# Performance work log

Measured on AMD Instinct MI355X. Metric: run time of the kernel, lower is better.

## Reference

```python
import jax, jax.numpy as jnp
import numpy as np

PATCH = 32        # max_patch_size == patch_stride == gate dim
LEVELS = 3        # n_real_experts; patch sizes 32 -> 16 -> 8
N_REAL = 3
N_NULL = 1
N_EXPERTS = N_REAL + N_NULL
K = 2             # n_activated_experts
ROUTE_SCALE = 1.0
SEQ_LEN = 2097152


def setup_inputs():
    key = jax.random.key(0)
    kx, kw = jax.random.split(key)
    x = jax.random.normal(kx, (1, SEQ_LEN), dtype=jnp.float32)
    mask = jnp.ones((1, SEQ_LEN), dtype=jnp.float32)
    Wg = jax.random.normal(kw, (N_EXPERTS, PATCH), dtype=jnp.float32) * 0.02
    return {"x": x, "mask": mask, "Wg": Wg}


def _route_structure(scores_np):
    """Concrete (non-differentiable) routing / split structure.
    scores_np: [P, E] gate softmax scores. Returns top-k ids, parent map,
    gather positions, validity mask, final sizes, granularity mask."""
    idx = np.argsort(-scores_np, axis=-1)[:, :K]                 # top-k expert ids [P,K]
    masked = np.where(idx < N_REAL, idx, -1)
    lvl = masked.max(axis=-1)
    lvl = np.maximum(lvl, 0)                                     # null-expert-only -> level 0
    counts = (1 << lvl).astype(np.int64)                         # each patch -> 2**lvl children
    P = scores_np.shape[0]
    total = int(counts.sum())
    parent = np.repeat(np.arange(P), counts)                     # [T] original patch id
    starts = np.cumsum(counts) - counts
    c = np.arange(total) - np.repeat(starts, counts)             # chunk index within parent
    v = lvl[parent]                                              # split level of each final patch
    sz = (PATCH >> v).astype(np.int64)                           # final patch length
    t = np.arange(PATCH)[None, :]
    valid = (t < sz[:, None])
    pos = np.where(valid, c[:, None] * sz[:, None] + t, 0)       # gather offsets in parent block
    # granularity mask: ones at own chunk at own level, and containing chunk one level coarser
    g = np.zeros((total, LEVELS, PATCH), np.float32)
    own = ((t >= (c * sz)[:, None]) & (t < ((c + 1) * sz)[:, None])).astype(np.float32)
    g[np.arange(total), v] = own
    hp = v >= 1
    szp = PATCH >> np.maximum(v - 1, 0)
    cp = c // 2
    par = ((t >= (cp * szp)[:, None]) & (t < ((cp + 1) * szp)[:, None])).astype(np.float32)
    g[np.arange(total)[hp], (v - 1)[hp]] = par[hp]
    return idx, parent, pos, valid, sz, g


def reference(x, mask, Wg):
    # non-overlapping patchify (stride == patch size)
    xp = x.reshape(-1, PATCH)                                    # [P, PATCH]
    mp = mask.reshape(-1, PATCH)
    scores = jax.nn.softmax(xp @ Wg.T, axis=-1)                  # [P, E] gate scores
    idx_np, parent, pos, valid, sz, g = _route_structure(np.asarray(scores))
    idx = jnp.asarray(idx_np)
    w_top = jnp.take_along_axis(scores, idx, axis=-1) * ROUTE_SCALE   # [P, K]
    parent_j = jnp.asarray(parent)
    pos_j = jnp.asarray(pos)
    valid_f = jnp.asarray(valid.astype(np.float32))
    xg = xp[parent_j]                                            # parent blocks [T, PATCH]
    mg = mp[parent_j]                                            # parent block masks
    new_x = jnp.take_along_axis(xg, pos_j, axis=1) * valid_f     # left-aligned, zero padded
    new_mask = jnp.take_along_axis(mg, pos_j, axis=1) * valid_f
    new_size = jnp.asarray(sz.astype(np.int32))                  # [T]
    weights = w_top[parent_j]                                    # children inherit routing [T,K]
    expert_idx = idx[parent_j]                                   # [T,K]
    gran = jnp.asarray(g)                                        # [T, LEVELS, PATCH]
    x_final = xg[:, None, :] * gran * mg[:, None, :]             # [T, LEVELS, PATCH]
    return (new_x[None], new_mask[None], new_size[None],
            weights[None], expert_idx[None], x_final[None])
```

## Files before the change

### kernel.cpp

```cpp
#include <hip/hip_runtime.h>

#define PATCH 32

__global__ __launch_bounds__(256) void k_gate(
    const float* __restrict__ x, const float* __restrict__ Wg,
    float* __restrict__ w0o, float* __restrict__ w1o,
    int* __restrict__ meta, int* __restrict__ lstart,
    int* __restrict__ blockSums)
{
    __shared__ float sx[256 * 33];
    __shared__ float sw[128];
    __shared__ int   sc[256];
    const int tid = threadIdx.x;
    const long base = (long)blockIdx.x * (256 * PATCH);

    for (int k = tid; k < 256 * PATCH; k += 256)
        sx[(k >> 5) * 33 + (k & 31)] = x[base + k];
    if (tid < 128) sw[tid] = Wg[tid];
    __syncthreads();

    const float* xp = &sx[tid * 33];
    float z0 = 0.f, z1 = 0.f, z2 = 0.f, z3 = 0.f;
    #pragma unroll
    for (int i = 0; i < 32; i++) {
        const float xv = xp[i];
        z0 = fmaf(xv, sw[i],      z0);
        z1 = fmaf(xv, sw[32 + i], z1);
        z2 = fmaf(xv, sw[64 + i], z2);
        z3 = fmaf(xv, sw[96 + i], z3);
    }
    const float zm = fmaxf(fmaxf(z0, z1), fmaxf(z2, z3));
    const float e0 = expf(z0 - zm), e1 = expf(z1 - zm),
                e2 = expf(z2 - zm), e3 = expf(z3 - zm);
    const float s = e0 + e1 + e2 + e3;
    float pv[4];
    pv[0] = e0 / s; pv[1] = e1 / s; pv[2] = e2 / s; pv[3] = e3 / s;

    int b0 = 0; float v0 = pv[0];
    #pragma unroll
    for (int i = 1; i < 4; i++) if (pv[i] > v0) { v0 = pv[i]; b0 = i; }
    int b1 = -1; float v1 = -1.f;
    #pragma unroll
    for (int i = 0; i < 4; i++) if (i != b0 && pv[i] > v1) { v1 = pv[i]; b1 = i; }

    const int m0 = (b0 < 3) ? b0 : -1;
    const int m1 = (b1 < 3) ? b1 : -1;
    int lv = m0 > m1 ? m0 : m1;
    if (lv < 0) lv = 0;
    const int cnt = 1 << lv;

    const int gp = blockIdx.x * 256 + tid;
    w0o[gp] = v0;
    w1o[gp] = v1;
    meta[gp] = b0 | (b1 << 4) | (lv << 8);

    sc[tid] = cnt;
    __syncthreads();
    for (int off = 1; off < 256; off <<= 1) {
        const int t = (tid >= off) ? sc[tid - off] : 0;
        __syncthreads();
        sc[tid] += t;
        __syncthreads();
    }
    lstart[gp] = sc[tid] - cnt;
    if (tid == 255) blockSums[blockIdx.x] = sc[255];
}

__global__ __launch_bounds__(256) void k_scan(
    const int* __restrict__ blockSums, int* __restrict__ blockOffs, int n)
{
    __shared__ int sc[256];
    const int tid = threadIdx.x;
    const int own = (tid < n) ? blockSums[tid] : 0;
    sc[tid] = own;
    __syncthreads();
    for (int off = 1; off < 256; off <<= 1) {
        const int t = (tid >= off) ? sc[tid - off] : 0;
        __syncthreads();
        sc[tid] += t;
        __syncthreads();
    }
    if (tid < n) blockOffs[tid] = sc[tid] - own;
}

__global__ __launch_bounds__(64) void k_emit(
    const float* __restrict__ x, const float* __restrict__ mask,
    const float* __restrict__ w0o, const float* __restrict__ w1o,
    const int* __restrict__ meta, const int* __restrict__ lstart,
    const int* __restrict__ blockOffs,
    float* __restrict__ o_newx, float* __restrict__ o_newm,
    float* __restrict__ o_size, float* __restrict__ o_w,
    float* __restrict__ o_eidx, float* __restrict__ o_xf)
{
    const int p = blockIdx.x;
    const int lane = threadIdx.x;
    __shared__ float shx[32], shm[32], shxm[32];
    if (lane < 32) {
        const float xv = x[(long)p * 32 + lane];
        const float mv = mask[(long)p * 32 + lane];
        shx[lane] = xv; shm[lane] = mv; shxm[lane] = xv * mv;
    }
    const int mt = meta[p];
    const int b0 = mt & 15, b1 = (mt >> 4) & 15, v = (mt >> 8) & 15;
    const int cnt = 1 << v, sz = 32 >> v;
    const long T0 = (long)blockOffs[p >> 8] + lstart[p];
    __syncthreads();

    const int n = cnt * 32;
    for (int j = lane; j < n; j += 64) {
        const int c = j >> 5, t = j & 31;
        const bool val = t < sz;
        const int src = val ? (c * sz + t) : 0;
        o_newx[T0 * 32 + j] = val ? shx[src] : 0.f;
        o_newm[T0 * 32 + j] = val ? shm[src] : 0.f;
    }

    const int nf = cnt * 96;
    for (int j = lane; j < nf; j += 64) {
        const int c = j / 96;
        const int rem = j - c * 96;
        const int l = rem >> 5, t = rem & 31;
        float val = 0.f;
        if (l == v) {
            const int lo = c * sz;
            if (t >= lo && t < lo + sz) val = shxm[t];
        } else if (v >= 1 && l == v - 1) {
            const int cp = c >> 1, szp = sz << 1;
            const int lo = cp * szp;
            if (t >= lo && t < lo + szp) val = shxm[t];
        }
        o_xf[T0 * 96 + j] = val;
    }

    if (lane < cnt) o_size[T0 + lane] = (float)sz;
    if (lane < 2 * cnt) {
        const int k = lane & 1;
        o_w[T0 * 2 + lane]    = k ? w1o[p] : w0o[p];
        o_eidx[T0 * 2 + lane] = (float)(k ? b1 : b0);
    }
}

extern "C" void kernel_launch(void* const* d_in, const int* in_sizes, int n_in,
                              void* d_out, int out_size, void* d_ws, size_t ws_size,
                              hipStream_t stream) {
    const float* x    = (const float*)d_in[0];
    const float* mask = (const float*)d_in[1];
    const float* Wg   = (const float*)d_in[2];

    const int  P  = in_sizes[0] / PATCH;
    const int  NB = (P + 255) / 256;
    const long T  = (long)out_size / 165;

    char* ws = (char*)d_ws;
    float* w0o = (float*)ws;  ws += (size_t)P * 4;
    float* w1o = (float*)ws;  ws += (size_t)P * 4;
    int*   meta = (int*)ws;   ws += (size_t)P * 4;
    int*   lst  = (int*)ws;   ws += (size_t)P * 4;
    int*   bsum = (int*)ws;   ws += (size_t)NB * 4;
    int*   boff = (int*)ws;

    float* out = (float*)d_out;
    float* o_newx = out;
    float* o_newm = out + T * 32;
    float* o_size = out + T * 64;
    float* o_w    = out + T * 65;
    float* o_eidx = out + T * 67;
    float* o_xf   = out + T * 69;

    hipLaunchKernelGGL(k_gate, dim3(NB), dim3(256), 0, stream,
                       x, Wg, w0o, w1o, meta, lst, bsum);
    hipLaunchKernelGGL(k_scan, dim3(1), dim3(256), 0, stream, bsum, boff, NB);
    hipLaunchKernelGGL(k_emit, dim3(P), dim3(64), 0, stream,
                       x, mask, w0o, w1o, meta, lst, boff,
                       o_newx, o_newm, o_size, o_w, o_eidx, o_xf);
}
```

Baseline: 165.3 us.

## Restructure emit into per-child rows with float4 stores and fused scan

The block-offset scan is folded into a new per-parent kernel that writes per-child metadata, sizes, weights and expert ids. The emit kernel now maps one 256-thread block to 32 output rows and writes newx, newm and x_final as coalesced float4 stores, instead of one 64-thread block per parent doing scalar writes. The gate kernel loads x directly into registers as float4 rather than staging through shared memory. This trades an extra child-metadata buffer, a redundant scan in every k_mid block, and an output-count-dependent grid for much better store coalescing and occupancy.

```diff
diff --git a/kernel.cpp b/kernel.cpp
--- a/kernel.cpp
+++ b/kernel.cpp
@@ -8,26 +8,31 @@
     int* __restrict__ meta, int* __restrict__ lstart,
     int* __restrict__ blockSums)
 {
-    __shared__ float sx[256 * 33];
     __shared__ float sw[128];
     __shared__ int   sc[256];
     const int tid = threadIdx.x;
-    const long base = (long)blockIdx.x * (256 * PATCH);
-
-    for (int k = tid; k < 256 * PATCH; k += 256)
-        sx[(k >> 5) * 33 + (k & 31)] = x[base + k];
     if (tid < 128) sw[tid] = Wg[tid];
-    __syncthreads();
-
-    const float* xp = &sx[tid * 33];
+
+    const long base = (long)blockIdx.x * (256 * PATCH) + (long)tid * PATCH;
+    const float4* xg = (const float4*)(x + base);
+    float4 xv[8];
+    #pragma unroll
+    for (int i = 0; i < 8; i++) xv[i] = xg[i];
+    __syncthreads();
+
     float z0 = 0.f, z1 = 0.f, z2 = 0.f, z3 = 0.f;
     #pragma unroll
-    for (int i = 0; i < 32; i++) {
-        const float xv = xp[i];
-        z0 = fmaf(xv, sw[i],      z0);
-        z1 = fmaf(xv, sw[32 + i], z1);
-        z2 = fmaf(xv, sw[64 + i], z2);
-        z3 = fmaf(xv, sw[96 + i], z3);
+    for (int i = 0; i < 8; i++) {
+        const float* f = (const float*)&xv[i];
+        #pragma unroll
+        for (int k = 0; k < 4; k++) {
+            const float v = f[k];
+            const int i4 = i * 4 + k;
+            z0 = fmaf(v, sw[i4],      z0);
+            z1 = fmaf(v, sw[32 + i4], z1);
+            z2 = fmaf(v, sw[64 + i4], z2);
+            z3 = fmaf(v, sw[96 + i4], z3);
+        }
     }
     const float zm = fmaxf(fmaxf(z0, z1), fmaxf(z2, z3));
     const float e0 = expf(z0 - zm), e1 = expf(z1 - zm),
@@ -66,77 +71,106 @@
     if (tid == 255) blockSums[blockIdx.x] = sc[255];
 }
 
-__global__ __launch_bounds__(256) void k_scan(
-    const int* __restrict__ blockSums, int* __restrict__ blockOffs, int n)
-{
-    __shared__ int sc[256];
-    const int tid = threadIdx.x;
-    const int own = (tid < n) ? blockSums[tid] : 0;
-    sc[tid] = own;
-    __syncthreads();
-    for (int off = 1; off < 256; off <<= 1) {
-        const int t = (tid >= off) ? sc[tid - off] : 0;
-        __syncthreads();
-        sc[tid] += t;
-        __syncthreads();
-    }
-    if (tid < n) blockOffs[tid] = sc[tid] - own;
-}
-
-__global__ __launch_bounds__(64) void k_emit(
-    const float* __restrict__ x, const float* __restrict__ mask,
+__global__ __launch_bounds__(256) void k_mid(
+    const int* __restrict__ blockSums,
     const float* __restrict__ w0o, const float* __restrict__ w1o,
     const int* __restrict__ meta, const int* __restrict__ lstart,
-    const int* __restrict__ blockOffs,
-    float* __restrict__ o_newx, float* __restrict__ o_newm,
+    int* __restrict__ childMeta,
     float* __restrict__ o_size, float* __restrict__ o_w,
-    float* __restrict__ o_eidx, float* __restrict__ o_xf)
+    float* __restrict__ o_eidx)
 {
-    const int p = blockIdx.x;
-    const int lane = threadIdx.x;
-    __shared__ float shx[32], shm[32], shxm[32];
-    if (lane < 32) {
-        const float xv = x[(long)p * 32 + lane];
-        const float mv = mask[(long)p * 32 + lane];
-        shx[lane] = xv; shm[lane] = mv; shxm[lane] = xv * mv;
-    }
+    __shared__ int sscan[256];
+    __shared__ int sOff;
+    const int tid = threadIdx.x;
+    const int own = blockSums[tid];
+    sscan[tid] = own;
+    __syncthreads();
+    for (int off = 1; off < 256; off <<= 1) {
+        const int t = (tid >= off) ? sscan[tid - off] : 0;
+        __syncthreads();
+        sscan[tid] += t;
+        __syncthreads();
+    }
+    if (tid == blockIdx.x) sOff = sscan[tid] - own;
+    __syncthreads();
+
+    const int p = blockIdx.x * 256 + tid;
     const int mt = meta[p];
     const int b0 = mt & 15, b1 = (mt >> 4) & 15, v = (mt >> 8) & 15;
-    const int cnt = 1 << v, sz = 32 >> v;
-    const long T0 = (long)blockOffs[p >> 8] + lstart[p];
-    __syncthreads();
-
-    const int n = cnt * 32;
-    for (int j = lane; j < n; j += 64) {
-        const int c = j >> 5, t = j & 31;
-        const bool val = t < sz;
-        const int src = val ? (c * sz + t) : 0;
-        o_newx[T0 * 32 + j] = val ? shx[src] : 0.f;
-        o_newm[T0 * 32 + j] = val ? shm[src] : 0.f;
-    }
-
-    const int nf = cnt * 96;
-    for (int j = lane; j < nf; j += 64) {
-        const int c = j / 96;
-        const int rem = j - c * 96;
-        const int l = rem >> 5, t = rem & 31;
-        float val = 0.f;
-        if (l == v) {
-            const int lo = c * sz;
-            if (t >= lo && t < lo + sz) val = shxm[t];
-        } else if (v >= 1 && l == v - 1) {
-            const int cp = c >> 1, szp = sz << 1;
-            const int lo = cp * szp;
-            if (t >= lo && t < lo + szp) val = shxm[t];
+    const int cnt = 1 << v, sz = PATCH >> v;
+    const long T0 = (long)sOff + lstart[p];
+    const float w0 = w0o[p], w1 = w1o[p];
+    const int packed = (p << 8) | (b0 << 6) | (b1 << 4) | v;
+    const float fsz = (float)sz, fb0 = (float)b0, fb1 = (float)b1;
+    for (int c = 0; c < cnt; c++) {
+        const long r = T0 + c;
+        childMeta[r] = packed | (c << 2);
+        o_size[r] = fsz;
+        o_w[r * 2]     = w0;  o_w[r * 2 + 1]     = w1;
+        o_eidx[r * 2]  = fb0; o_eidx[r * 2 + 1]  = fb1;
+    }
+}
+
+__global__ __launch_bounds__(256) void k_emit(
+    const float* __restrict__ x, const float* __restrict__ mask,
+    const int* __restrict__ childMeta, const long T,
+    float4* __restrict__ o_newx, float4* __restrict__ o_newm,
+    float4* __restrict__ o_xf)
+{
+    __shared__ int smeta[32];
+    const int tid = threadIdx.x;
+    const long R0 = (long)blockIdx.x * 32;
+    if (tid < 32) smeta[tid] = (R0 + tid < T) ? childMeta[R0 + tid] : 0;
+    __syncthreads();
+
+    {
+        const int j = tid >> 3, q = tid & 7;
+        const long r = R0 + j;
+        if (r < T) {
+            const int m = smeta[j];
+            const int p = m >> 8, c = (m >> 2) & 3, v = m & 3;
+            const int sz = PATCH >> v;
+            float4 vx = {0.f, 0.f, 0.f, 0.f}, vm = {0.f, 0.f, 0.f, 0.f};
+            if (4 * q < sz) {
+                const long src = (long)p * PATCH + c * sz + 4 * q;
+                vx = *(const float4*)(x + src);
+                vm = *(const float4*)(mask + src);
+            }
+            o_newx[r * 8 + q] = vx;
+            o_newm[r * 8 + q] = vm;
         }
-        o_xf[T0 * 96 + j] = val;
-    }
-
-    if (lane < cnt) o_size[T0 + lane] = (float)sz;
-    if (lane < 2 * cnt) {
-        const int k = lane & 1;
-        o_w[T0 * 2 + lane]    = k ? w1o[p] : w0o[p];
-        o_eidx[T0 * 2 + lane] = (float)(k ? b1 : b0);
+    }
+
+    #pragma unroll
+    for (int it = 0; it < 3; it++) {
+        const int f = it * 256 + tid;
+        const int j = f / 24;
+        const int rem = f - j * 24;
+        const int l = rem >> 3, q = rem & 7;
+        const long r = R0 + j;
+        if (r < T) {
+            const int m = smeta[j];
+            const int p = m >> 8, c = (m >> 2) & 3, v = m & 3;
+            const int sz = PATCH >> v;
+            const int t4 = 4 * q;
+            bool nz = false;
+            if (l == v) {
+                const int lo = c * sz;
+                nz = (t4 >= lo) && (t4 < lo + sz);
+            } else if (v >= 1 && l == v - 1) {
+                const int cp = c >> 1, szp = sz << 1, lo = cp * szp;
+                nz = (t4 >= lo) && (t4 < lo + szp);
+            }
+            float4 out = {0.f, 0.f, 0.f, 0.f};
+            if (nz) {
+                const long src = (long)p * PATCH + t4;
+                const float4 vx = *(const float4*)(x + src);
+                const float4 vm = *(const float4*)(mask + src);
+                out.x = vx.x * vm.x; out.y = vx.y * vm.y;
+                out.z = vx.z * vm.z; out.w = vx.w * vm.w;
+            }
+            o_xf[r * 24 + l * 8 + q] = out;
+        }
     }
 }
 
@@ -152,12 +186,12 @@
     const long T  = (long)out_size / 165;
 
     char* ws = (char*)d_ws;
-    float* w0o = (float*)ws;  ws += (size_t)P * 4;
-    float* w1o = (float*)ws;  ws += (size_t)P * 4;
-    int*   meta = (int*)ws;   ws += (size_t)P * 4;
-    int*   lst  = (int*)ws;   ws += (size_t)P * 4;
-    int*   bsum = (int*)ws;   ws += (size_t)NB * 4;
-    int*   boff = (int*)ws;
+    float* w0o  = (float*)ws;  ws += (size_t)P * 4;
+    float* w1o  = (float*)ws;  ws += (size_t)P * 4;
+    int*   meta = (int*)ws;    ws += (size_t)P * 4;
+    int*   lst  = (int*)ws;    ws += (size_t)P * 4;
+    int*   bsum = (int*)ws;    ws += (size_t)NB * 4;
+    int*   cmeta = (int*)ws;
 
     float* out = (float*)d_out;
     float* o_newx = out;
@@ -169,8 +203,10 @@
 
     hipLaunchKernelGGL(k_gate, dim3(NB), dim3(256), 0, stream,
                        x, Wg, w0o, w1o, meta, lst, bsum);
-    hipLaunchKernelGGL(k_scan, dim3(1), dim3(256), 0, stream, bsum, boff, NB);
-    hipLaunchKernelGGL(k_emit, dim3(P), dim3(64), 0, stream,
-                       x, mask, w0o, w1o, meta, lst, boff,
-                       o_newx, o_newm, o_size, o_w, o_eidx, o_xf);
-}
+    hipLaunchKernelGGL(k_mid, dim3(NB), dim3(256), 0, stream,
+                       bsum, w0o, w1o, meta, lst, cmeta, o_size, o_w, o_eidx);
+    const int NE = (int)((T + 31) / 32);
+    hipLaunchKernelGGL(k_emit, dim3(NE), dim3(256), 0, stream,
+                       x, mask, cmeta, T,
+                       (float4*)o_newx, (float4*)o_newm, (float4*)o_xf);
+}
```

Result: faster. 151.2 us (-8.6%).

## Fuse gate, scan and emit into single kernel with decoupled lookback

Applied to the files above, without the earlier changes.

Replaces the three-kernel pipeline (gate, single-block scan, per-patch emit) with one fused kernel. Each block computes gate scores, does a local prefix scan, publishes its block sum through a ready-flagged atomic, and sums predecessor flags by spinning on them. It then writes all outputs for its 256 patches using vectorized float4 non-temporal stores, with rows mapped through shared memory. This removes workspace round trips, two launches, and the 65536 tiny emit blocks. The cost is a serial spin-wait dependency across blocks, plus a memset of the flags before launch.

```diff
diff --git a/kernel.cpp b/kernel.cpp
--- a/kernel.cpp
+++ b/kernel.cpp
@@ -1,33 +1,55 @@
 #include <hip/hip_runtime.h>
 
 #define PATCH 32
+#define FLAGRDY (1 << 30)
+#define SUMMASK 0xFFFFFF
 
-__global__ __launch_bounds__(256) void k_gate(
-    const float* __restrict__ x, const float* __restrict__ Wg,
-    float* __restrict__ w0o, float* __restrict__ w1o,
-    int* __restrict__ meta, int* __restrict__ lstart,
-    int* __restrict__ blockSums)
+typedef float f4 __attribute__((ext_vector_type(4)));
+
+__device__ __forceinline__ f4 to_f4(const float4 v) {
+    f4 r; r.x = v.x; r.y = v.y; r.z = v.z; r.w = v.w; return r;
+}
+
+__global__ __launch_bounds__(256) void k_fused(
+    const float* __restrict__ x, const float* __restrict__ mask,
+    const float* __restrict__ Wg,
+    int* __restrict__ flags,
+    float* __restrict__ o_newx, float* __restrict__ o_newm,
+    float* __restrict__ o_size, float* __restrict__ o_w,
+    float* __restrict__ o_eidx, float* __restrict__ o_xf)
 {
-    __shared__ float sx[256 * 33];
     __shared__ float sw[128];
     __shared__ int   sc[256];
+    __shared__ int   sMeta[256];
+    __shared__ float sW0[256], sW1[256];
+    __shared__ int   sRowP[1024];
+    __shared__ int   sOffS;
+
     const int tid = threadIdx.x;
-    const long base = (long)blockIdx.x * (256 * PATCH);
+    const int bid = blockIdx.x;
+    if (tid < 128) sw[tid] = Wg[tid];
 
-    for (int k = tid; k < 256 * PATCH; k += 256)
-        sx[(k >> 5) * 33 + (k & 31)] = x[base + k];
-    if (tid < 128) sw[tid] = Wg[tid];
+    const long pbase = (long)bid * (256 * PATCH);
+    const float4* x4 = (const float4*)(x + pbase);
+    const float4* m4 = (const float4*)(mask + pbase);
+    float4 xv[8];
+    #pragma unroll
+    for (int i = 0; i < 8; i++) xv[i] = x4[tid * 8 + i];
     __syncthreads();
 
-    const float* xp = &sx[tid * 33];
     float z0 = 0.f, z1 = 0.f, z2 = 0.f, z3 = 0.f;
     #pragma unroll
-    for (int i = 0; i < 32; i++) {
-        const float xv = xp[i];
-        z0 = fmaf(xv, sw[i],      z0);
-        z1 = fmaf(xv, sw[32 + i], z1);
-        z2 = fmaf(xv, sw[64 + i], z2);
-        z3 = fmaf(xv, sw[96 + i], z3);
+    for (int i = 0; i < 8; i++) {
+        const float4 f = xv[i];
+        const int i4 = i * 4;
+        z0 = fmaf(f.x, sw[i4],      z0); z0 = fmaf(f.y, sw[i4+1],      z0);
+        z0 = fmaf(f.z, sw[i4+2],    z0); z0 = fmaf(f.w, sw[i4+3],      z0);
+        z1 = fmaf(f.x, sw[32+i4],   z1); z1 = fmaf(f.y, sw[32+i4+1],   z1);
+        z1 = fmaf(f.z, sw[32+i4+2], z1); z1 = fmaf(f.w, sw[32+i4+3],   z1);
+        z2 = fmaf(f.x, sw[64+i4],   z2); z2 = fmaf(f.y, sw[64+i4+1],   z2);
+        z2 = fmaf(f.z, sw[64+i4+2], z2); z2 = fmaf(f.w, sw[64+i4+3],   z2);
+        z3 = fmaf(f.x, sw[96+i4],   z3); z3 = fmaf(f.y, sw[96+i4+1],   z3);
+        z3 = fmaf(f.z, sw[96+i4+2], z3); z3 = fmaf(f.w, sw[96+i4+3],   z3);
     }
     const float zm = fmaxf(fmaxf(z0, z1), fmaxf(z2, z3));
     const float e0 = expf(z0 - zm), e1 = expf(z1 - zm),
@@ -49,10 +71,9 @@
     if (lv < 0) lv = 0;
     const int cnt = 1 << lv;
 
-    const int gp = blockIdx.x * 256 + tid;
-    w0o[gp] = v0;
-    w1o[gp] = v1;
-    meta[gp] = b0 | (b1 << 4) | (lv << 8);
+    sMeta[tid] = b0 | (b1 << 4) | (lv << 8);
+    sW0[tid] = v0;
+    sW1[tid] = v1;
 
     sc[tid] = cnt;
     __syncthreads();
@@ -62,81 +83,90 @@
         sc[tid] += t;
         __syncthreads();
     }
-    lstart[gp] = sc[tid] - cnt;
-    if (tid == 255) blockSums[blockIdx.x] = sc[255];
-}
+    const int lst = sc[tid] - cnt;
 
-__global__ __launch_bounds__(256) void k_scan(
-    const int* __restrict__ blockSums, int* __restrict__ blockOffs, int n)
-{
-    __shared__ int sc[256];
-    const int tid = threadIdx.x;
-    const int own = (tid < n) ? blockSums[tid] : 0;
-    sc[tid] = own;
-    __syncthreads();
-    for (int off = 1; off < 256; off <<= 1) {
-        const int t = (tid >= off) ? sc[tid - off] : 0;
-        __syncthreads();
-        sc[tid] += t;
-        __syncthreads();
+    if (tid == 255)
+        __hip_atomic_store(&flags[bid], FLAGRDY | sc[255],
+                           __ATOMIC_RELAXED, __HIP_MEMORY_SCOPE_AGENT);
+
+    for (int c = 0; c < cnt; c++) sRowP[lst + c] = (tid << 2) | c;
+
+    if (tid < 64) {
+        int acc = 0;
+        for (int b = tid; b < bid; b += 64) {
+            int f;
+            while ((((f = __hip_atomic_load(&flags[b], __ATOMIC_RELAXED,
+                                            __HIP_MEMORY_SCOPE_AGENT))) & FLAGRDY) == 0)
+                __builtin_amdgcn_s_sleep(4);
+            acc += f & SUMMASK;
+        }
+        #pragma unroll
+        for (int off = 32; off >= 1; off >>= 1) acc += __shfl_down(acc, off);
+        if (tid == 0) sOffS = acc;
     }
-    if (tid < n) blockOffs[tid] = sc[tid] - own;
-}
-
-__global__ __launch_bounds__(64) void k_emit(
-    const float* __restrict__ x, const float* __restrict__ mask,
-    const float* __restrict__ w0o, const float* __restrict__ w1o,
-    const int* __restrict__ meta, const int* __restrict__ lstart,
-    const int* __restrict__ blockOffs,
-    float* __restrict__ o_newx, float* __restrict__ o_newm,
-    float* __restrict__ o_size, float* __restrict__ o_w,
-    float* __restrict__ o_eidx, float* __restrict__ o_xf)
-{
-    const int p = blockIdx.x;
-    const int lane = threadIdx.x;
-    __shared__ float shx[32], shm[32], shxm[32];
-    if (lane < 32) {
-        const float xv = x[(long)p * 32 + lane];
-        const float mv = mask[(long)p * 32 + lane];
-        shx[lane] = xv; shm[lane] = mv; shxm[lane] = xv * mv;
-    }
-    const int mt = meta[p];
-    const int b0 = mt & 15, b1 = (mt >> 4) & 15, v = (mt >> 8) & 15;
-    const int cnt = 1 << v, sz = 32 >> v;
-    const long T0 = (long)blockOffs[p >> 8] + lstart[p];
     __syncthreads();
 
-    const int n = cnt * 32;
-    for (int j = lane; j < n; j += 64) {
-        const int c = j >> 5, t = j & 31;
-        const bool val = t < sz;
-        const int src = val ? (c * sz + t) : 0;
-        o_newx[T0 * 32 + j] = val ? shx[src] : 0.f;
-        o_newm[T0 * 32 + j] = val ? shm[src] : 0.f;
+    const int  bs = sc[255];
+    const long R0 = sOffS;
+
+    for (int g = tid; g < bs; g += 256) {
+        const int jp = sRowP[g] >> 2;
+        const int v = (sMeta[jp] >> 8) & 15;
+        __builtin_nontemporal_store((float)(PATCH >> v), &o_size[R0 + g]);
+    }
+    for (int g = tid; g < 2 * bs; g += 256) {
+        const int row = g >> 1, k = g & 1;
+        const int jp = sRowP[row] >> 2;
+        const int mt = sMeta[jp];
+        const float wv = k ? sW1[jp] : sW0[jp];
+        const float ev = (float)(k ? ((mt >> 4) & 15) : (mt & 15));
+        __builtin_nontemporal_store(wv, &o_w[R0 * 2 + g]);
+        __builtin_nontemporal_store(ev, &o_eidx[R0 * 2 + g]);
     }
 
-    const int nf = cnt * 96;
-    for (int j = lane; j < nf; j += 64) {
-        const int c = j / 96;
-        const int rem = j - c * 96;
-        const int l = rem >> 5, t = rem & 31;
-        float val = 0.f;
+    f4* __restrict__ onx = (f4*)o_newx + R0 * 8;
+    f4* __restrict__ onm = (f4*)o_newm + R0 * 8;
+    for (int g = tid; g < bs * 8; g += 256) {
+        const int row = g >> 3, q = g & 7;
+        const int rp = sRowP[row];
+        const int jp = rp >> 2, c = rp & 3;
+        const int sz = PATCH >> ((sMeta[jp] >> 8) & 15);
+        f4 vx = {0.f, 0.f, 0.f, 0.f}, vm = {0.f, 0.f, 0.f, 0.f};
+        if (4 * q < sz) {
+            const int off = jp * 8 + ((c * sz) >> 2) + q;
+            vx = to_f4(x4[off]);
+            vm = to_f4(m4[off]);
+        }
+        __builtin_nontemporal_store(vx, &onx[g]);
+        __builtin_nontemporal_store(vm, &onm[g]);
+    }
+
+    f4* __restrict__ oxf = (f4*)o_xf + R0 * 24;
+    for (int g = tid; g < bs * 24; g += 256) {
+        const int row = g / 24;
+        const int rem = g - row * 24;
+        const int l = rem >> 3, q = rem & 7;
+        const int rp = sRowP[row];
+        const int jp = rp >> 2, c = rp & 3;
+        const int v = (sMeta[jp] >> 8) & 15;
+        const int sz = PATCH >> v;
+        const int t4 = 4 * q;
+        bool nz = false;
         if (l == v) {
             const int lo = c * sz;
-            if (t >= lo && t < lo + sz) val = shxm[t];
+            nz = (t4 >= lo) && (t4 < lo + sz);
         } else if (v >= 1 && l == v - 1) {
-            const int cp = c >> 1, szp = sz << 1;
-            const int lo = cp * szp;
-            if (t >= lo && t < lo + szp) val = shxm[t];
+            const int cp = c >> 1, szp = sz << 1, lo = cp * szp;
+            nz = (t4 >= lo) && (t4 < lo + szp);
         }
-        o_xf[T0 * 96 + j] = val;
-    }
-
-    if (lane < cnt) o_size[T0 + lane] = (float)sz;
-    if (lane < 2 * cnt) {
-        const int k = lane & 1;
-        o_w[T0 * 2 + lane]    = k ? w1o[p] : w0o[p];
-        o_eidx[T0 * 2 + lane] = (float)(k ? b1 : b0);
+        f4 o = {0.f, 0.f, 0.f, 0.f};
+        if (nz) {
+            const int off = jp * 8 + q;
+            const float4 a = x4[off], b = m4[off];
+            o.x = a.x * b.x; o.y = a.y * b.y;
+            o.z = a.z * b.z; o.w = a.w * b.w;
+        }
+        __builtin_nontemporal_store(o, &oxf[g]);
     }
 }
 
@@ -151,13 +181,7 @@
     const int  NB = (P + 255) / 256;
     const long T  = (long)out_size / 165;
 
-    char* ws = (char*)d_ws;
-    float* w0o = (float*)ws;  ws += (size_t)P * 4;
-    float* w1o = (float*)ws;  ws += (size_t)P * 4;
-    int*   meta = (int*)ws;   ws += (size_t)P * 4;
-    int*   lst  = (int*)ws;   ws += (size_t)P * 4;
-    int*   bsum = (int*)ws;   ws += (size_t)NB * 4;
-    int*   boff = (int*)ws;
+    int* flags = (int*)d_ws;
 
     float* out = (float*)d_out;
     float* o_newx = out;
@@ -167,10 +191,8 @@
     float* o_eidx = out + T * 67;
     float* o_xf   = out + T * 69;
 
-    hipLaunchKernelGGL(k_gate, dim3(NB), dim3(256), 0, stream,
-                       x, Wg, w0o, w1o, meta, lst, bsum);
-    hipLaunchKernelGGL(k_scan, dim3(1), dim3(256), 0, stream, bsum, boff, NB);
-    hipLaunchKernelGGL(k_emit, dim3(P), dim3(64), 0, stream,
-                       x, mask, w0o, w1o, meta, lst, boff,
+    (void)hipMemsetAsync(flags, 0, (size_t)NB * sizeof(int), stream);
+    hipLaunchKernelGGL(k_fused, dim3(NB), dim3(256), 0, stream,
+                       x, mask, Wg, flags,
                        o_newx, o_newm, o_size, o_w, o_eidx, o_xf);
 }
```

Result: slower. 175.1 us (+5.9%).
